# Kernel tuning notes

Hardware: AMD Instinct MI355X
Metric: run time of the kernel (lower is better)

The kernel has to match this reference:

```python
import jax, jax.numpy as jnp
import numpy as np

N, M, F_IN, F_OUT, B = 8192, 4096, 256, 128, 2048
NEG = -9e15
EPS = 1e-5


def leaky(x, slope=0.2):
    return jnp.where(x > 0, x, slope * x)


def batchnorm(x, gamma, beta):
    # BatchNorm1d training-mode semantics: biased batch stats over dim 0
    m = x.mean(axis=0)
    v = jnp.var(x, axis=0)
    return (x - m) * jax.lax.rsqrt(v + EPS) * gamma + beta


def setup_inputs() -> dict:
    key = jax.random.key(0)
    ks = jax.random.split(key, 12)
    inp = {}
    inp["Sinput"] = jax.random.normal(ks[0], (N, F_IN), dtype=jnp.float32)
    inp["Rinput"] = jax.random.normal(ks[1], (M, F_IN), dtype=jnp.float32)
    inp["inter_adj"] = jax.random.randint(ks[2], (N, M), 0, 2).astype(jnp.int32)
    inp["city_adj"] = jax.random.randint(ks[3], (N, N), 0, 2).astype(jnp.int32)
    inp["province_adj"] = jax.random.randint(ks[4], (N, N), 0, 2).astype(jnp.int32)
    inp["source_index"] = jax.random.randint(ks[5], (B,), 0, N).astype(jnp.int32)
    s_w = 1.414 * np.sqrt(6.0 / (F_IN + F_OUT))  # xavier_uniform gain=1.414
    s_a = 1.414 * np.sqrt(6.0 / (2 * F_OUT + 1))
    inp["W1"] = jax.random.uniform(ks[6], (F_IN, F_OUT), jnp.float32, -s_w, s_w)
    inp["W2"] = jax.random.uniform(ks[7], (F_IN, F_OUT), jnp.float32, -s_w, s_w)
    inp["a"] = jax.random.uniform(ks[8], (2 * F_OUT, 1), jnp.float32, -s_a, s_a)
    inp["a3"] = jax.random.uniform(ks[9], (2 * F_OUT, 1), jnp.float32, -s_a, s_a)
    inp["a4"] = jax.random.uniform(ks[10], (2 * F_OUT, 1), jnp.float32, -s_a, s_a)
    inp["bn1_gamma"] = jnp.ones((F_OUT,), jnp.float32)
    inp["bn1_beta"] = jnp.zeros((F_OUT,), jnp.float32)
    inp["bn2_gamma"] = jnp.ones((F_OUT,), jnp.float32)
    inp["bn2_beta"] = jnp.zeros((F_OUT,), jnp.float32)
    return inp


def reference(Sinput, Rinput, inter_adj, city_adj, province_adj, source_index,
              W1, W2, a, a3, a4, bn1_gamma, bn1_beta, bn2_gamma, bn2_beta):
    F = W1.shape[1]
    h1 = Rinput @ W1            # [M, F]
    h2 = Sinput @ W2            # [N, F]
    # Decomposed GAT score: cat([h1[m], h2[n]]) @ a == h1[m]@a[:F] + h2[n]@a[F:]
    e12 = leaky((h2 @ a[F:, 0])[:, None] + (h1 @ a[:F, 0])[None, :])  # [N, M]
    att_inter = jax.nn.softmax(jnp.where(inter_adj > 0, e12, NEG), axis=1)
    h2_ = h2[source_index]      # [B, F]
    # cat([h2_, h2_]) @ a3 -> h2_ @ (a3[:F] + a3[F:]), constant along N axis
    s3 = leaky(h2_ @ (a3[:F, 0] + a3[F:, 0]))  # [B]
    s4 = leaky(h2_ @ (a4[:F, 0] + a4[F:, 0]))  # [B]
    Nn = Sinput.shape[0]
    e3 = jnp.broadcast_to(s3[:, None], (s3.shape[0], Nn))
    e4 = jnp.broadcast_to(s4[:, None], (s4.shape[0], Nn))
    att3 = jax.nn.softmax(jnp.where(city_adj[source_index] > 0, e3, NEG), axis=1)
    att4 = jax.nn.softmax(jnp.where(province_adj[source_index] > 0, e4, NEG), axis=1)
    InterRC = att_inter @ h1                    # [N, F]
    IntraNC = att3.T @ h2_ + att4.T @ h2_       # [N, F]
    v_output = leaky(batchnorm(att_inter.T @ h2, bn1_gamma, bn1_beta))  # [M, F]
    u_output = leaky(batchnorm(InterRC + IntraNC, bn2_gamma, bn2_beta))  # [N, F]
    h_prime = u_output @ v_output.T             # [N, M]
    return jax.nn.elu(h_prime)
```

## Files before the change

kernel.cpp:

```cpp
#include <hip/hip_runtime.h>
#include <stdint.h>

#define N_ 8192
#define M_ 4096
#define FIN_ 256
#define F_ 128
#define B_ 2048

typedef __attribute__((ext_vector_type(8))) short vs8;
typedef __attribute__((ext_vector_type(8))) __bf16 vb8;
typedef __attribute__((ext_vector_type(4))) float vf4;

union ABu { vs8 s; vb8 b; };

__device__ __forceinline__ vf4 mfma16(const ABu& a, const ABu& b, vf4 c) {
    return __builtin_amdgcn_mfma_f32_16x16x32_bf16(a.b, b.b, c, 0, 0, 0);
}
__device__ __forceinline__ unsigned short f2b(float x) {
    union { float f; unsigned u; } v; v.f = x;
    unsigned r = v.u + 0x7fffu + ((v.u >> 16) & 1u);
    return (unsigned short)(r >> 16);
}
__device__ __forceinline__ float lrelu(float x) { return x > 0.f ? x : 0.2f * x; }

__global__ void k_prep(const float* __restrict__ W1, const float* __restrict__ W2,
                       unsigned short* __restrict__ W1T, unsigned short* __restrict__ W2T,
                       float4* __restrict__ Z, int nz4) {
    int id = blockIdx.x * 256 + threadIdx.x;
    if (id < 65536) {
        const float* W = (id < 32768) ? W1 : W2;
        unsigned short* WT = (id < 32768) ? W1T : W2T;
        int o = id & 32767;
        int f = o >> 8, k = o & 255;
        WT[o] = f2b(W[k * F_ + f]);
    } else {
        int z = id - 65536;
        if (z < nz4) Z[z] = make_float4(0.f, 0.f, 0.f, 0.f);
    }
}

__global__ __launch_bounds__(256) void k_hgemmF(const float* __restrict__ Rin, const float* __restrict__ Sin,
                                                const unsigned short* __restrict__ W1T,
                                                const unsigned short* __restrict__ W2T,
                                                const float* __restrict__ a,
                                                float* __restrict__ h2,
                                                unsigned short* __restrict__ h1P, unsigned short* __restrict__ h2P,
                                                float* __restrict__ s1, float* __restrict__ s2) {
    __shared__ unsigned short tb[16][136];
    __shared__ float sred[4][16];
    int t = threadIdx.x;
    int w = t >> 6, l = t & 63, lr = l & 15, lg = l >> 4;
    int gr = blockIdx.x * 16;
    const float* X; const unsigned short* WT; unsigned short* HP; float* sout; const float* av;
    int row0; bool isH2;
    if (gr < M_) { X = Rin; WT = W1T; HP = h1P; sout = s1; av = a;      row0 = gr;      isH2 = false; }
    else         { X = Sin; WT = W2T; HP = h2P; sout = s2; av = a + F_; row0 = gr - M_; isH2 = true;  }
    int fbase = w * 32;
    vf4 acc[2] = {};
    const float* xp = X + (size_t)(row0 + lr) * FIN_ + lg * 8;
#pragma unroll
    for (int kk = 0; kk < FIN_; kk += 32) {
        float4 xa = *(const float4*)(xp + kk);
        float4 xb = *(const float4*)(xp + kk + 4);
        ABu af;
        af.s[0] = (short)f2b(xa.x); af.s[1] = (short)f2b(xa.y);
        af.s[2] = (short)f2b(xa.z); af.s[3] = (short)f2b(xa.w);
        af.s[4] = (short)f2b(xb.x); af.s[5] = (short)f2b(xb.y);
        af.s[6] = (short)f2b(xb.z); af.s[7] = (short)f2b(xb.w);
#pragma unroll
        for (int q = 0; q < 2; ++q) {
            ABu bf; bf.s = *(const vs8*)(WT + (fbase + q * 16 + lr) * FIN_ + kk + lg * 8);
            acc[q] = mfma16(af, bf, acc[q]);
        }
    }
    if (isH2) {
#pragma unroll
        for (int q = 0; q < 2; ++q)
#pragma unroll
            for (int r = 0; r < 4; ++r)
                h2[(size_t)(row0 + lg * 4 + r) * F_ + fbase + q * 16 + lr] = acc[q][r];
    }
#pragma unroll
    for (int q = 0; q < 2; ++q)
#pragma unroll
        for (int r = 0; r < 4; ++r)
            tb[lg * 4 + r][fbase + q * 16 + lr] = f2b(acc[q][r]);
    float a0 = av[fbase + lr], a1 = av[fbase + 16 + lr];
    float tv[4];
#pragma unroll
    for (int r = 0; r < 4; ++r) tv[r] = acc[0][r] * a0 + acc[1][r] * a1;
#pragma unroll
    for (int off = 1; off < 16; off <<= 1)
#pragma unroll
        for (int r = 0; r < 4; ++r) tv[r] += __shfl_xor(tv[r], off, 64);
    if ((l & 15) == 0)
#pragma unroll
        for (int r = 0; r < 4; ++r) sred[w][lg * 4 + r] = tv[r];
    __syncthreads();
    {
        int f = t >> 1, half = t & 1;
        vs8 o;
#pragma unroll
        for (int j = 0; j < 8; ++j) o[j] = (short)tb[half * 8 + j][f];
        *(vs8*)(HP + ((size_t)(row0 >> 5) * 128 + f) * 32 + (row0 & 16) + half * 8) = o;
    }
    if (t < 16) {
        float s = sred[0][t] + sred[1][t] + sred[2][t] + sred[3][t];
        sout[row0 + t] = s;
    }
}

__global__ __launch_bounds__(256) void k_adjgather(const int* __restrict__ inter, const float* __restrict__ s1,
                                                   const float* __restrict__ s2, unsigned short* __restrict__ bm,
                                                   float* __restrict__ rowmax, float* __restrict__ rowinv,
                                                   const int* __restrict__ city, const int* __restrict__ prov,
                                                   const int* __restrict__ src,
                                                   uint32_t* __restrict__ BMtc, uint32_t* __restrict__ BMtp,
                                                   float* __restrict__ w3, float* __restrict__ w4,
                                                   const float* __restrict__ h2, unsigned short* __restrict__ h2wP) {
    __shared__ float wred[8];
    int t = threadIdx.x;
    int wv = t >> 6, ln = t & 63;
    if (blockIdx.x < N_) {
        int n = blockIdx.x;
        const int* rp = inter + (size_t)n * M_ + t * 16;
        float sv[16]; unsigned mask = 0;
#pragma unroll
        for (int c = 0; c < 4; ++c) {
            int4 v = *(const int4*)(rp + c * 4);
            if (v.x > 0) mask |= 1u << (c * 4 + 0);
            if (v.y > 0) mask |= 1u << (c * 4 + 1);
            if (v.z > 0) mask |= 1u << (c * 4 + 2);
            if (v.w > 0) mask |= 1u << (c * 4 + 3);
            float4 s = *(const float4*)(s1 + t * 16 + c * 4);
            sv[c * 4 + 0] = s.x; sv[c * 4 + 1] = s.y; sv[c * 4 + 2] = s.z; sv[c * 4 + 3] = s.w;
        }
        bm[(size_t)n * 256 + t] = (unsigned short)(mask & 0xffffu);
        float mx = -3.0e38f;
#pragma unroll
        for (int j = 0; j < 16; ++j) if (mask & (1u << j)) mx = fmaxf(mx, sv[j]);
        for (int off = 32; off > 0; off >>= 1) mx = fmaxf(mx, __shfl_down(mx, off, 64));
        if (ln == 0) wred[wv] = mx;
        __syncthreads();
        float s1mx = fmaxf(fmaxf(wred[0], wred[1]), fmaxf(wred[2], wred[3]));
        float s2n = s2[n];
        float rmx = lrelu(s2n + s1mx);
        float sum = 0.f;
#pragma unroll
        for (int j = 0; j < 16; ++j) if (mask & (1u << j)) sum += __expf(lrelu(s2n + sv[j]) - rmx);
        for (int off = 32; off > 0; off >>= 1) sum += __shfl_down(sum, off, 64);
        if (ln == 0) wred[4 + wv] = sum;
        __syncthreads();
        if (t == 0) {
            float tot = wred[4] + wred[5] + wred[6] + wred[7];
            bool any = s1mx > -2.9e38f;
            rowmax[n] = any ? rmx : 0.f;
            rowinv[n] = (any && tot > 0.f) ? 1.0f / tot : 0.f;
        }
    } else if (blockIdx.x < N_ + 2 * B_) {
        int bb = blockIdx.x - N_;
        int b = bb & (B_ - 1);
        bool isC = bb < B_;
        const int* adj = isC ? city : prov;
        uint32_t* BM = isC ? BMtc : BMtp;
        float* wout = isC ? w3 : w4;
        const int* rowp = adj + (size_t)src[b] * N_;
        int cnt = 0;
#pragma unroll 4
        for (int i = 0; i < N_ / 256; ++i) {
            int v = rowp[i * 256 + t];
            unsigned long long bal = __ballot(v > 0);
            cnt += (v > 0);
            if (ln == 0) {
                int widx = i * 8 + wv * 2;
                BM[(size_t)widx * B_ + b] = (uint32_t)bal;
                BM[(size_t)(widx + 1) * B_ + b] = (uint32_t)(bal >> 32);
            }
        }
        float fc = (float)cnt;
        for (int off = 32; off > 0; off >>= 1) fc += __shfl_down(fc, off, 64);
        if (ln == 0) wred[wv] = fc;
        __syncthreads();
        if (t == 0) {
            float tot = wred[0] + wred[1] + wred[2] + wred[3];
            wout[b] = tot > 0.f ? 1.0f / tot : 0.f;
        }
    } else {
        int bblk = blockIdx.x - (N_ + 2 * B_);
        int f = t & 127, halfb = t >> 7;
        vs8 o0, o1;
#pragma unroll
        for (int i = 0; i < 8; ++i) {
            int b0 = bblk * 32 + halfb * 16 + i;
            o0[i] = (short)f2b(h2[(size_t)src[b0] * F_ + f]);
            int b1 = b0 + 8;
            o1[i] = (short)f2b(h2[(size_t)src[b1] * F_ + f]);
        }
        unsigned short* dst = h2wP + ((size_t)bblk * 128 + f) * 32 + halfb * 16;
        *(vs8*)dst = o0;
        *(vs8*)(dst + 8) = o1;
    }
}

__global__ __launch_bounds__(256) void k_attmat(const unsigned char* __restrict__ bm8,
                                                const float* __restrict__ s1, const float* __restrict__ s2,
                                                const float* __restrict__ rowmax, const float* __restrict__ rowinv,
                                                unsigned short* __restrict__ attP) {
    int tid = blockIdx.x * 256 + threadIdx.x;
    int moct = tid & 3;
    int n = (tid >> 2) & (N_ - 1);
    int mblk = tid >> 15;
    int m = mblk * 32 + moct * 8;
    unsigned bits = bm8[(size_t)n * 512 + (m >> 3)];
    float s2n = s2[n], rmx = rowmax[n], rin = rowinv[n];
    float4 sa = *(const float4*)(s1 + m);
    float4 sb = *(const float4*)(s1 + m + 4);
    float sv[8] = {sa.x, sa.y, sa.z, sa.w, sb.x, sb.y, sb.z, sb.w};
    vs8 o;
#pragma unroll
    for (int j = 0; j < 8; ++j) {
        float v = (bits & (1u << j)) ? __expf(lrelu(s2n + sv[j]) - rmx) * rin : 0.f;
        o[j] = (short)f2b(v);
    }
    *(vs8*)(attP + ((size_t)mblk * N_ + n) * 32 + moct * 8) = o;
}

__global__ __launch_bounds__(256) void k_gemmABC(const unsigned short* __restrict__ attP,
                                                 const unsigned short* __restrict__ h1P,
                                                 const unsigned short* __restrict__ h2P,
                                                 const uint32_t* __restrict__ BMtc, const uint32_t* __restrict__ BMtp,
                                                 const float* __restrict__ w3, const float* __restrict__ w4,
                                                 const unsigned short* __restrict__ h2wP,
                                                 float* __restrict__ u_in, float* __restrict__ v_in) {
    __shared__ unsigned short lds[32][34];
    int t = threadIdx.x;
    int w = t >> 6, l = t & 63;
    int lr = l & 15, lg = l >> 4;
    int bx = blockIdx.x;
    if (bx < 1024) {
        int xa = bx & 255, ya = bx >> 8;
        int nb = xa * 32 + (w >> 1) * 16;
        int fb = (w & 1) * 64;
        vf4 acc[4] = {};
        for (int mblk = ya * 32; mblk < ya * 32 + 32; ++mblk) {
            ABu af; af.s = *(const vs8*)(attP + ((size_t)mblk * N_ + nb + lr) * 32 + lg * 8);
#pragma unroll
            for (int q = 0; q < 4; ++q) {
                ABu bf; bf.s = *(const vs8*)(h1P + ((size_t)mblk * 128 + fb + q * 16 + lr) * 32 + lg * 8);
                acc[q] = mfma16(af, bf, acc[q]);
            }
        }
#pragma unroll
        for (int q = 0; q < 4; ++q)
#pragma unroll
            for (int r = 0; r < 4; ++r)
                atomicAdd(&u_in[(size_t)(nb + lg * 4 + r) * F_ + fb + q * 16 + lr], acc[q][r]);
    } else if (bx < 1536) {
        int i = bx - 1024;
        int xb = i & 127, yb = i >> 7;
        int mb = xb * 32;
        int mh = (w >> 1) * 16;
        int fb = (w & 1) * 64;
        int si = t >> 3;
        int sc = (t & 7) * 4;
        vf4 acc[4] = {};
        const unsigned short* abase = attP + (size_t)(mb >> 5) * N_ * 32;
        int n0s = yb * (N_ / 4);
        for (int n0 = n0s; n0 < n0s + N_ / 4; n0 += 32) {
            uint2 dv = *(const uint2*)(abase + (size_t)(n0 + si) * 32 + sc);
            __syncthreads();
            lds[sc + 0][si] = (unsigned short)(dv.x & 0xffffu);
            lds[sc + 1][si] = (unsigned short)(dv.x >> 16);
            lds[sc + 2][si] = (unsigned short)(dv.y & 0xffffu);
            lds[sc + 3][si] = (unsigned short)(dv.y >> 16);
            __syncthreads();
            ABu af; af.s = *(const vs8*)&lds[mh + lr][lg * 8];
#pragma unroll
            for (int q = 0; q < 4; ++q) {
                ABu bf; bf.s = *(const vs8*)(h2P + ((size_t)(n0 >> 5) * 128 + fb + q * 16 + lr) * 32 + lg * 8);
                acc[q] = mfma16(af, bf, acc[q]);
            }
        }
#pragma unroll
        for (int q = 0; q < 4; ++q)
#pragma unroll
            for (int r = 0; r < 4; ++r)
                atomicAdd(&v_in[(size_t)(mb + mh + lg * 4 + r) * F_ + fb + q * 16 + lr], acc[q][r]);
    } else {
        int i = bx - 1536;
        int xc = i & 255, yc = i >> 8;
        int nb = xc * 32 + (w >> 1) * 16;
        int fb = (w & 1) * 64;
        int n = nb + lr;
        int wi = n >> 5;
        int bitpos = n & 31;
        const uint32_t* bc = BMtc + (size_t)wi * B_;
        const uint32_t* bp = BMtp + (size_t)wi * B_;
        vf4 acc[4] = {};
        int b0s = yc * (B_ / 2);
        for (int b0 = b0s; b0 < b0s + B_ / 2; b0 += 32) {
            int bb = b0 + lg * 8;
            uint4 c0 = *(const uint4*)(bc + bb);
            uint4 c1 = *(const uint4*)(bc + bb + 4);
            uint4 p0 = *(const uint4*)(bp + bb);
            uint4 p1 = *(const uint4*)(bp + bb + 4);
            float4 wa = *(const float4*)(w3 + bb);
            float4 wb = *(const float4*)(w3 + bb + 4);
            float4 wc = *(const float4*)(w4 + bb);
            float4 wd = *(const float4*)(w4 + bb + 4);
            uint32_t cw[8] = {c0.x, c0.y, c0.z, c0.w, c1.x, c1.y, c1.z, c1.w};
            uint32_t pw[8] = {p0.x, p0.y, p0.z, p0.w, p1.x, p1.y, p1.z, p1.w};
            float w3v[8] = {wa.x, wa.y, wa.z, wa.w, wb.x, wb.y, wb.z, wb.w};
            float w4v[8] = {wc.x, wc.y, wc.z, wc.w, wd.x, wd.y, wd.z, wd.w};
            ABu af;
#pragma unroll
            for (int j = 0; j < 8; ++j) {
                float v = (((cw[j] >> bitpos) & 1u) ? w3v[j] : 0.f) + (((pw[j] >> bitpos) & 1u) ? w4v[j] : 0.f);
                af.s[j] = (short)f2b(v);
            }
#pragma unroll
            for (int q = 0; q < 4; ++q) {
                ABu bf; bf.s = *(const vs8*)(h2wP + ((size_t)(b0 >> 5) * 128 + fb + q * 16 + lr) * 32 + lg * 8);
                acc[q] = mfma16(af, bf, acc[q]);
            }
        }
#pragma unroll
        for (int q = 0; q < 4; ++q)
#pragma unroll
            for (int r = 0; r < 4; ++r)
                atomicAdd(&u_in[(size_t)(nb + lg * 4 + r) * F_ + fb + q * 16 + lr], acc[q][r]);
    }
}

__global__ __launch_bounds__(256) void k_bnstats2(const float* __restrict__ v_in, const float* __restrict__ u_in,
                                                  float* __restrict__ stats) {
    __shared__ float r1[256], r2[256];
    int bx = blockIdx.x;
    const float* P; int R; float* sum; float* sq;
    if (bx < 128) { P = v_in; R = M_; sum = stats;       sq = stats + 128; }
    else          { P = u_in; R = N_; sum = stats + 256; sq = stats + 384; bx -= 128; }
    int f = threadIdx.x & 127;
    int half = threadIdx.x >> 7;
    float s = 0.f, s2v = 0.f;
    for (int r = bx * 2 + half; r < R; r += 256) {
        float v = P[(size_t)r * F_ + f];
        s += v; s2v += v * v;
    }
    r1[threadIdx.x] = s; r2[threadIdx.x] = s2v;
    __syncthreads();
    if (half == 0) {
        atomicAdd(&sum[f], r1[f] + r1[f + 128]);
        atomicAdd(&sq[f], r2[f] + r2[f + 128]);
    }
}

__global__ __launch_bounds__(256) void k_bnapplyF(const float* __restrict__ v_in, const float* __restrict__ u_in,
                                                  const float* __restrict__ stats,
                                                  const float* __restrict__ g1, const float* __restrict__ b1,
                                                  const float* __restrict__ g2, const float* __restrict__ b2,
                                                  unsigned short* __restrict__ v_outb, unsigned short* __restrict__ u_outb) {
    __shared__ float sc[256], sh[256];
    int t = threadIdx.x;
    {
        int which = t >> 7, f = t & 127;
        const float* sum = stats + which * 256;
        const float* sq = sum + 128;
        const float* g = which ? g2 : g1;
        const float* be = which ? b2 : b1;
        float R = which ? (float)N_ : (float)M_;
        float mean = sum[f] / R;
        float var = sq[f] / R - mean * mean;
        float s = g[f] * rsqrtf(var + 1e-5f);
        sc[t] = s; sh[t] = be[f] - mean * s;
    }
    __syncthreads();
    int id4 = blockIdx.x * 256 + t;
    int idx = id4 * 4;
    int which = idx >= M_ * F_;
    int rel = which ? idx - M_ * F_ : idx;
    const float* P = which ? u_in : v_in;
    unsigned short* Q = which ? u_outb : v_outb;
    int f0 = (rel & 127) + which * 128;
    float4 p = *(const float4*)(P + rel);
    ushort4 o;
    o.x = f2b(lrelu(p.x * sc[f0 + 0] + sh[f0 + 0]));
    o.y = f2b(lrelu(p.y * sc[f0 + 1] + sh[f0 + 1]));
    o.z = f2b(lrelu(p.z * sc[f0 + 2] + sh[f0 + 2]));
    o.w = f2b(lrelu(p.w * sc[f0 + 3] + sh[f0 + 3]));
    *(ushort4*)(Q + rel) = o;
}

__global__ __launch_bounds__(256) void k_gemmD(const unsigned short* __restrict__ U,
                                               const unsigned short* __restrict__ V,
                                               float* __restrict__ out) {
    int w = threadIdx.x >> 6, l = threadIdx.x & 63;
    int lr = l & 15, lg = l >> 4;
    int nb = blockIdx.x * 64 + w * 16;
    int mb = blockIdx.y * 64;
    vf4 acc[4] = {};
#pragma unroll
    for (int k0 = 0; k0 < F_; k0 += 32) {
        ABu af; af.s = *(const vs8*)(U + (size_t)(nb + lr) * F_ + k0 + lg * 8);
#pragma unroll
        for (int q = 0; q < 4; ++q) {
            ABu bf; bf.s = *(const vs8*)(V + (size_t)(mb + q * 16 + lr) * F_ + k0 + lg * 8);
            acc[q] = mfma16(af, bf, acc[q]);
        }
    }
#pragma unroll
    for (int q = 0; q < 4; ++q)
#pragma unroll
        for (int r = 0; r < 4; ++r) {
            int row = nb + lg * 4 + r;
            int col = mb + q * 16 + lr;
            float x = acc[q][r];
            out[(size_t)row * M_ + col] = x > 0.f ? x : __expf(x) - 1.f;
        }
}

extern "C" void kernel_launch(void* const* d_in, const int* in_sizes, int n_in,
                              void* d_out, int out_size, void* d_ws, size_t ws_size,
                              hipStream_t stream) {
    const float* Sinput = (const float*)d_in[0];
    const float* Rinput = (const float*)d_in[1];
    const int* inter_adj = (const int*)d_in[2];
    const int* city_adj = (const int*)d_in[3];
    const int* prov_adj = (const int*)d_in[4];
    const int* src = (const int*)d_in[5];
    const float* W1 = (const float*)d_in[6];
    const float* W2 = (const float*)d_in[7];
    const float* a = (const float*)d_in[8];
    const float* g1 = (const float*)d_in[11];
    const float* b1 = (const float*)d_in[12];
    const float* g2 = (const float*)d_in[13];
    const float* b2 = (const float*)d_in[14];
    float* out = (float*)d_out;

    char* ws = (char*)d_ws;
    size_t o = 0;
    auto take = [&](size_t bytes) { char* p = ws + o; o += (bytes + 255) & ~(size_t)255; return p; };
    float* u_in = (float*)take((size_t)N_ * F_ * 4);
    float* v_in = (float*)take((size_t)M_ * F_ * 4);
    float* stats = (float*)take(512 * 4);
    size_t zero_bytes = o;
    float* h2 = (float*)take((size_t)N_ * F_ * 4);
    unsigned short* h1P = (unsigned short*)take((size_t)(M_ / 32) * 128 * 32 * 2);
    unsigned short* h2P = (unsigned short*)take((size_t)(N_ / 32) * 128 * 32 * 2);
    unsigned short* W1T = (unsigned short*)take((size_t)F_ * FIN_ * 2);
    unsigned short* W2T = (unsigned short*)take((size_t)F_ * FIN_ * 2);
    float* s1 = (float*)take(M_ * 4);
    float* s2 = (float*)take(N_ * 4);
    float* rowmax = (float*)take(N_ * 4);
    float* rowinv = (float*)take(N_ * 4);
    float* w3 = (float*)take(B_ * 4);
    float* w4 = (float*)take(B_ * 4);
    unsigned short* h2wP = (unsigned short*)take((size_t)(B_ / 32) * 128 * 32 * 2);
    unsigned short* u_outb = (unsigned short*)take((size_t)N_ * F_ * 2);
    unsigned short* v_outb = (unsigned short*)take((size_t)M_ * F_ * 2);
    uint32_t* BMtc = (uint32_t*)take((size_t)256 * B_ * 4);
    uint32_t* BMtp = (uint32_t*)take((size_t)256 * B_ * 4);
    unsigned short* bm = (unsigned short*)take((size_t)N_ * 256 * 2);
    unsigned short* attP = (unsigned short*)take((size_t)N_ * M_ * 2);
    (void)ws_size; (void)in_sizes; (void)n_in; (void)out_size;

    int nz4 = (int)(zero_bytes / 16);
    int zblocks = (nz4 + 255) / 256;
    k_prep<<<256 + zblocks, 256, 0, stream>>>(W1, W2, W1T, W2T, (float4*)d_ws, nz4);
    k_hgemmF<<<(M_ + N_) / 16, 256, 0, stream>>>(Rinput, Sinput, W1T, W2T, a, h2, h1P, h2P, s1, s2);
    k_adjgather<<<N_ + 2 * B_ + B_ / 32, 256, 0, stream>>>(inter_adj, s1, s2, bm, rowmax, rowinv,
                                                           city_adj, prov_adj, src, BMtc, BMtp, w3, w4,
                                                           h2, h2wP);
    k_attmat<<<16384, 256, 0, stream>>>((const unsigned char*)bm, s1, s2, rowmax, rowinv, attP);
    k_gemmABC<<<2048, 256, 0, stream>>>(attP, h1P, h2P, BMtc, BMtp, w3, w4, h2wP, u_in, v_in);
    k_bnstats2<<<256, 256, 0, stream>>>(v_in, u_in, stats);
    k_bnapplyF<<<(M_ + N_) * F_ / 4 / 256, 256, 0, stream>>>(v_in, u_in, stats, g1, b1, g2, b2, v_outb, u_outb);
    k_gemmD<<<dim3(N_ / 64, M_ / 64), 256, 0, stream>>>(u_outb, v_outb, out);
}
```

Measured before the change: 352.1 us.

## Retile fused attention GEMMs for register reuse and wider LDS transpose staging

Restructures the three sub-GEMMs inside the fused attention kernel. The att@h1 and mask@h2w parts now have each wave compute two 16-row tiles that share every B fragment, which halves B loads per MFMA; their grids are re-split so they cover the same work. The att^T@h2 part now stages 128 columns per LDS transpose and runs four K-steps per barrier pair instead of one, cutting synchronisation and using 16-byte global loads, with more split-K blocks. The aim is less global-load and barrier overhead per MFMA, at the cost of more registers, a larger LDS tile with possible bank conflicts on the scalar transposed stores, and more atomics for the v_in path.

After: 359.5 us. 2.1% more time.

```diff
diff --git a/kernel.cpp b/kernel.cpp
--- a/kernel.cpp
+++ b/kernel.cpp
@@ -232,53 +232,64 @@
                                                  const float* __restrict__ w3, const float* __restrict__ w4,
                                                  const unsigned short* __restrict__ h2wP,
                                                  float* __restrict__ u_in, float* __restrict__ v_in) {
-    __shared__ unsigned short lds[32][34];
+    __shared__ unsigned short lds3[32][136];
     int t = threadIdx.x;
     int w = t >> 6, l = t & 63;
     int lr = l & 15, lg = l >> 4;
     int bx = blockIdx.x;
     if (bx < 1024) {
-        int xa = bx & 255, ya = bx >> 8;
-        int nb = xa * 32 + (w >> 1) * 16;
-        int fb = (w & 1) * 64;
-        vf4 acc[4] = {};
-        for (int mblk = ya * 32; mblk < ya * 32 + 32; ++mblk) {
-            ABu af; af.s = *(const vs8*)(attP + ((size_t)mblk * N_ + nb + lr) * 32 + lg * 8);
+        int xa = bx & 127, ya = bx >> 7;
+        int nb0 = xa * 64 + (w & 1) * 32;
+        int fb = (w >> 1) * 64;
+        vf4 acc[2][4] = {};
+        for (int mblk = ya * 16; mblk < ya * 16 + 16; ++mblk) {
+            const unsigned short* ab = attP + ((size_t)mblk * N_ + nb0 + lr) * 32 + lg * 8;
+            ABu af0, af1;
+            af0.s = *(const vs8*)ab;
+            af1.s = *(const vs8*)(ab + 16 * 32);
 #pragma unroll
             for (int q = 0; q < 4; ++q) {
                 ABu bf; bf.s = *(const vs8*)(h1P + ((size_t)mblk * 128 + fb + q * 16 + lr) * 32 + lg * 8);
-                acc[q] = mfma16(af, bf, acc[q]);
+                acc[0][q] = mfma16(af0, bf, acc[0][q]);
+                acc[1][q] = mfma16(af1, bf, acc[1][q]);
             }
         }
 #pragma unroll
-        for (int q = 0; q < 4; ++q)
-#pragma unroll
-            for (int r = 0; r < 4; ++r)
-                atomicAdd(&u_in[(size_t)(nb + lg * 4 + r) * F_ + fb + q * 16 + lr], acc[q][r]);
-    } else if (bx < 1536) {
+        for (int s = 0; s < 2; ++s)
+#pragma unroll
+            for (int q = 0; q < 4; ++q)
+#pragma unroll
+                for (int r = 0; r < 4; ++r)
+                    atomicAdd(&u_in[(size_t)(nb0 + s * 16 + lg * 4 + r) * F_ + fb + q * 16 + lr], acc[s][q][r]);
+    } else if (bx < 2048) {
         int i = bx - 1024;
         int xb = i & 127, yb = i >> 7;
         int mb = xb * 32;
-        int mh = (w >> 1) * 16;
-        int fb = (w & 1) * 64;
-        int si = t >> 3;
-        int sc = (t & 7) * 4;
+        int mh = (w & 1) * 16;
+        int fb = (w >> 1) * 64;
         vf4 acc[4] = {};
-        const unsigned short* abase = attP + (size_t)(mb >> 5) * N_ * 32;
-        int n0s = yb * (N_ / 4);
-        for (int n0 = n0s; n0 < n0s + N_ / 4; n0 += 32) {
-            uint2 dv = *(const uint2*)(abase + (size_t)(n0 + si) * 32 + sc);
+        const unsigned short* abase = attP + (size_t)xb * N_ * 32;
+        int stg = t >> 1, shalf = t & 1;
+        for (int c = 0; c < 8; ++c) {
+            int n0 = yb * 1024 + c * 128;
+            const unsigned short* srcp = abase + (size_t)n0 * 32 + t * 16;
+            vs8 d0 = *(const vs8*)srcp;
+            vs8 d1 = *(const vs8*)(srcp + 8);
             __syncthreads();
-            lds[sc + 0][si] = (unsigned short)(dv.x & 0xffffu);
-            lds[sc + 1][si] = (unsigned short)(dv.x >> 16);
-            lds[sc + 2][si] = (unsigned short)(dv.y & 0xffffu);
-            lds[sc + 3][si] = (unsigned short)(dv.y >> 16);
+#pragma unroll
+            for (int j = 0; j < 8; ++j) lds3[shalf * 16 + j][stg] = (unsigned short)d0[j];
+#pragma unroll
+            for (int j = 0; j < 8; ++j) lds3[shalf * 16 + 8 + j][stg] = (unsigned short)d1[j];
             __syncthreads();
-            ABu af; af.s = *(const vs8*)&lds[mh + lr][lg * 8];
-#pragma unroll
-            for (int q = 0; q < 4; ++q) {
-                ABu bf; bf.s = *(const vs8*)(h2P + ((size_t)(n0 >> 5) * 128 + fb + q * 16 + lr) * 32 + lg * 8);
-                acc[q] = mfma16(af, bf, acc[q]);
+#pragma unroll
+            for (int kc = 0; kc < 4; ++kc) {
+                ABu af; af.s = *(const vs8*)&lds3[mh + lr][kc * 32 + lg * 8];
+                int nblk = (n0 >> 5) + kc;
+#pragma unroll
+                for (int q = 0; q < 4; ++q) {
+                    ABu bf; bf.s = *(const vs8*)(h2P + ((size_t)nblk * 128 + fb + q * 16 + lr) * 32 + lg * 8);
+                    acc[q] = mfma16(af, bf, acc[q]);
+                }
             }
         }
 #pragma unroll
@@ -287,18 +298,16 @@
             for (int r = 0; r < 4; ++r)
                 atomicAdd(&v_in[(size_t)(mb + mh + lg * 4 + r) * F_ + fb + q * 16 + lr], acc[q][r]);
     } else {
-        int i = bx - 1536;
-        int xc = i & 255, yc = i >> 8;
-        int nb = xc * 32 + (w >> 1) * 16;
-        int fb = (w & 1) * 64;
-        int n = nb + lr;
-        int wi = n >> 5;
-        int bitpos = n & 31;
+        int i = bx - 2048;
+        int xc = i & 127, yc = i >> 7;
+        int nb0 = xc * 64 + (w & 1) * 32;
+        int fb = (w >> 1) * 64;
+        int wi = nb0 >> 5;
         const uint32_t* bc = BMtc + (size_t)wi * B_;
         const uint32_t* bp = BMtp + (size_t)wi * B_;
-        vf4 acc[4] = {};
-        int b0s = yc * (B_ / 2);
-        for (int b0 = b0s; b0 < b0s + B_ / 2; b0 += 32) {
+        vf4 acc[2][4] = {};
+        int b0s = yc * (B_ / 4);
+        for (int b0 = b0s; b0 < b0s + B_ / 4; b0 += 32) {
             int bb = b0 + lg * 8;
             uint4 c0 = *(const uint4*)(bc + bb);
             uint4 c1 = *(const uint4*)(bc + bb + 4);
@@ -312,23 +321,28 @@
             uint32_t pw[8] = {p0.x, p0.y, p0.z, p0.w, p1.x, p1.y, p1.z, p1.w};
             float w3v[8] = {wa.x, wa.y, wa.z, wa.w, wb.x, wb.y, wb.z, wb.w};
             float w4v[8] = {wc.x, wc.y, wc.z, wc.w, wd.x, wd.y, wd.z, wd.w};
-            ABu af;
+            ABu af0, af1;
 #pragma unroll
             for (int j = 0; j < 8; ++j) {
-                float v = (((cw[j] >> bitpos) & 1u) ? w3v[j] : 0.f) + (((pw[j] >> bitpos) & 1u) ? w4v[j] : 0.f);
-                af.s[j] = (short)f2b(v);
+                float v0 = (((cw[j] >> lr) & 1u) ? w3v[j] : 0.f) + (((pw[j] >> lr) & 1u) ? w4v[j] : 0.f);
+                float v1 = (((cw[j] >> (16 + lr)) & 1u) ? w3v[j] : 0.f) + (((pw[j] >> (16 + lr)) & 1u) ? w4v[j] : 0.f);
+                af0.s[j] = (short)f2b(v0);
+                af1.s[j] = (short)f2b(v1);
             }
 #pragma unroll
             for (int q = 0; q < 4; ++q) {
                 ABu bf; bf.s = *(const vs8*)(h2wP + ((size_t)(b0 >> 5) * 128 + fb + q * 16 + lr) * 32 + lg * 8);
-                acc[q] = mfma16(af, bf, acc[q]);
+                acc[0][q] = mfma16(af0, bf, acc[0][q]);
+                acc[1][q] = mfma16(af1, bf, acc[1][q]);
             }
         }
 #pragma unroll
-        for (int q = 0; q < 4; ++q)
-#pragma unroll
-            for (int r = 0; r < 4; ++r)
-                atomicAdd(&u_in[(size_t)(nb + lg * 4 + r) * F_ + fb + q * 16 + lr], acc[q][r]);
+        for (int s = 0; s < 2; ++s)
+#pragma unroll
+            for (int q = 0; q < 4; ++q)
+#pragma unroll
+                for (int r = 0; r < 4; ++r)
+                    atomicAdd(&u_in[(size_t)(nb0 + s * 16 + lg * 4 + r) * F_ + fb + q * 16 + lr], acc[s][q][r]);
     }
 }
 
@@ -471,7 +485,7 @@
                                                            city_adj, prov_adj, src, BMtc, BMtp, w3, w4,
                                                            h2, h2wP);
     k_attmat<<<16384, 256, 0, stream>>>((const unsigned char*)bm, s1, s2, rowmax, rowinv, attP);
-    k_gemmABC<<<2048, 256, 0, stream>>>(attP, h1P, h2P, BMtc, BMtp, w3, w4, h2wP, u_in, v_in);
+    k_gemmABC<<<2560, 256, 0, stream>>>(attP, h1P, h2P, BMtc, BMtp, w3, w4, h2wP, u_in, v_in);
     k_bnstats2<<<256, 256, 0, stream>>>(v_in, u_in, stats);
     k_bnapplyF<<<(M_ + N_) * F_ / 4 / 256, 256, 0, stream>>>(v_in, u_in, stats, g1, b1, g2, b2, v_outb, u_outb);
     k_gemmD<<<dim3(N_ / 64, M_ / 64), 256, 0, stream>>>(u_outb, v_outb, out);
```
